# Kernel optimization log

Measured on AMD Instinct MI355X. Metric: run time of the kernel, lower is better.

The kernel has to match this reference:

```python
import jax, jax.numpy as jnp
import numpy as np

N_GENE, N_TRAIN, E = 2500, 16384, 4194304
SRC_DIM, DST_DIM, HID, OUT, NCLS = 2500, 2675, 2500, 2500, 16


def setup_inputs() -> dict:
    key = jax.random.key(0)
    ks = jax.random.split(key, 16)
    s = 0.02
    return {
        "gene_feat": jax.random.normal(ks[0], (N_GENE, SRC_DIM), jnp.float32),
        "train_feat": jax.random.normal(ks[1], (N_TRAIN, DST_DIM), jnp.float32),
        "edge_src": jax.random.randint(ks[2], (E,), 0, N_GENE, jnp.int32),
        "edge_dst": jax.random.randint(ks[3], (E,), 0, N_TRAIN, jnp.int32),
        # conv1: SAGEConv((src=2500, dst=2675) -> 2500, mean)
        "W1_self": jax.random.normal(ks[4], (HID, DST_DIM), jnp.float32) * s,
        "W1_neigh": jax.random.normal(ks[5], (HID, SRC_DIM), jnp.float32) * s,
        "b1": jnp.zeros((HID,), jnp.float32),
        # conv2: SAGEConv(2500 -> 2500, mean); src feats are original gene feats
        "W2_self": jax.random.normal(ks[6], (OUT, HID), jnp.float32) * s,
        "W2_neigh": jax.random.normal(ks[7], (OUT, SRC_DIM), jnp.float32) * s,
        "b2": jnp.zeros((OUT,), jnp.float32),
        # classifier MLP
        "Wc1": jax.random.normal(ks[8], (OUT, OUT), jnp.float32) * s,
        "bc1": jnp.zeros((OUT,), jnp.float32),
        "Wc2": jax.random.normal(ks[9], (NCLS, OUT), jnp.float32) * s,
        "bc2": jnp.zeros((NCLS,), jnp.float32),
    }


def reference(gene_feat, train_feat, edge_src, edge_dst,
              W1_self, W1_neigh, b1, W2_self, W2_neigh, b2,
              Wc1, bc1, Wc2, bc2):
    # Dense incidence-count matrix A[dst, src]: # edges between (dst, src).
    # mean-aggregation over in-edges == (A @ gene_feat) / in_degree.
    A = jnp.zeros((N_TRAIN, N_GENE), jnp.float32).at[edge_dst, edge_src].add(1.0)
    deg = jnp.maximum(A.sum(axis=1, keepdims=True), 1.0)  # zero-in-deg -> neigh term = 0
    mean_src = (A @ gene_feat) / deg                      # [N_train, 2500]

    # conv1 ('connects'): fc_self(dst) + fc_neigh(mean(src)) + bias; then ReLU
    h = jax.nn.relu(train_feat @ W1_self.T + mean_src @ W1_neigh.T + b1)

    # conv2: dst feats = h, src feats = original gene_feat (same graph)
    h2 = jax.nn.relu(h @ W2_self.T + mean_src @ W2_neigh.T + b2)

    # classifier MLP
    return jax.nn.relu(h2 @ Wc1.T + bc1) @ Wc2.T + bc2   # [N_train, 16]
```

## Files before the change

kernel.cpp:

```cpp
#include <hip/hip_runtime.h>
#include <stdint.h>

typedef unsigned short u16;
typedef unsigned int u32;
typedef __attribute__((ext_vector_type(4))) float f32x4;
typedef __attribute__((ext_vector_type(8))) short bf16x8;

#define MROWS 16384
#define NP    2560
#define K1P   2688


__device__ __forceinline__ u16 f2bf(float f) {
    u32 u = __float_as_uint(f);
    u32 r = (u + 0x7fffu + ((u >> 16) & 1u)) >> 16;
    return (u16)r;
}

__device__ __forceinline__ void async_ld16(const void* g, void* l) {
    __builtin_amdgcn_global_load_lds((const __attribute__((address_space(1))) u32*)g,
                                     (__attribute__((address_space(3))) u32*)l,
                                     16, 0, 0);
}


__global__ void cvt_pad(const float* __restrict__ src, u16* __restrict__ dst,
                        int R, int C, int Cp) {
    const int r = blockIdx.x;
    u16* drow = dst + (size_t)r * Cp;
    if (r < R) {
        const float* srow = src + (size_t)r * C;
        for (int c = threadIdx.x; c < Cp; c += blockDim.x)
            drow[c] = (c < C) ? f2bf(srow[c]) : (u16)0;
    } else {
        for (int c = threadIdx.x; c < Cp; c += blockDim.x) drow[c] = 0;
    }
}

__global__ void pad_vec(const float* __restrict__ src, float* __restrict__ dst,
                        int n, int np) {
    int i = blockIdx.x * blockDim.x + threadIdx.x;
    if (i < np) dst[i] = (i < n) ? src[i] : 0.f;
}

__global__ void transpose_cvt(const float* __restrict__ src, u16* __restrict__ dst) {
    __shared__ float t[64][65];
    const int n0 = blockIdx.x * 64;
    const int k0 = blockIdx.y * 64;
    const int tx = threadIdx.x, ty = threadIdx.y;
    for (int i = ty; i < 64; i += 4) {
        int k = k0 + i, n = n0 + tx;
        t[i][tx] = (k < 2500 && n < 2500) ? src[(size_t)k * 2500 + n] : 0.f;
    }
    __syncthreads();
    for (int i = ty; i < 64; i += 4)
        dst[(size_t)(n0 + i) * NP + k0 + tx] = f2bf(t[tx][i]);
}

__global__ void build_counts(const int* __restrict__ esrc, const int* __restrict__ edst,
                             int E, float* __restrict__ acnt) {
    int i = blockIdx.x * blockDim.x + threadIdx.x;
    if (i < E) atomicAdd(&acnt[(size_t)edst[i] * NP + esrc[i]], 1.0f);
}

__global__ void row_rdeg(const float* __restrict__ acnt, float* __restrict__ rdeg) {
    const int row = blockIdx.x;
    const float4* p = (const float4*)(acnt + (size_t)row * NP);
    float s = 0.f;
    for (int i = threadIdx.x; i < NP / 4; i += 64) {
        float4 v = p[i];
        s += v.x + v.y + v.z + v.w;
    }
    #pragma unroll
    for (int off = 32; off > 0; off >>= 1) s += __shfl_down(s, off, 64);
    if (threadIdx.x == 0) rdeg[row] = 1.f / fmaxf(s, 1.f);
}

template<bool PAIR2, bool BIAS_RELU>
__global__ __launch_bounds__(256) void gemm_bt(
    const u16* __restrict__ A1, const u16* __restrict__ B1, int K1,
    const u16* __restrict__ A2, const u16* __restrict__ B2, int K2,
    const float* __restrict__ epi, u16* __restrict__ C, int N)
{
    __shared__ __align__(16) u16 lA[128 * 64];
    __shared__ __align__(16) u16 lB[128 * 64];

    const int tid  = threadIdx.x;
    const int bm   = blockIdx.y * 128;
    const int bn   = blockIdx.x * 128;
    const int wave = tid >> 6;
    const int lane = tid & 63;
    const int wr   = (wave >> 1) << 6;
    const int wc   = (wave & 1) << 6;
    const int lrow = lane & 15;
    const int lkq  = lane >> 4;
    const int xr   = lrow & 7;

    const int sr  = tid >> 3;
    const int sc  = (tid & 7) << 3;
    const int gsw = (((tid & 7) ^ (sr & 7)) << 3);

    f32x4 acc[4][4] = {};

    #pragma unroll
    for (int pair = 0; pair < (PAIR2 ? 2 : 1); ++pair) {
        const u16* A = (PAIR2 && pair) ? A2 : A1;
        const u16* B = (PAIR2 && pair) ? B2 : B1;
        const int  K = (PAIR2 && pair) ? K2 : K1;
        const u16* gA = A + (size_t)(bm + sr) * K + gsw;
        const u16* gB = B + (size_t)(bn + sr) * K + gsw;
        u16* sA = lA + sr * 64 + sc;
        u16* sB = lB + sr * 64 + sc;
        const int nkt = K >> 6;
        for (int kt = 0; kt < nkt; ++kt) {
            __syncthreads();
            const u16* ga = gA + kt * 64;
            const u16* gb = gB + kt * 64;
            #pragma unroll
            for (int i = 0; i < 4; ++i)
                async_ld16(ga + (size_t)i * 32 * K, sA + i * 32 * 64);
            #pragma unroll
            for (int i = 0; i < 4; ++i)
                async_ld16(gb + (size_t)i * 32 * K, sB + i * 32 * 64);
            __syncthreads();
            #pragma unroll
            for (int ks = 0; ks < 2; ++ks) {
                bf16x8 af[4], bfr[4];
                #pragma unroll
                for (int i = 0; i < 4; ++i)
                    af[i] = *(const bf16x8*)(lA + (wr + i * 16 + lrow) * 64 +
                                             (((ks * 4 + lkq) ^ xr) << 3));
                #pragma unroll
                for (int i = 0; i < 4; ++i)
                    bfr[i] = *(const bf16x8*)(lB + (wc + i * 16 + lrow) * 64 +
                                              (((ks * 4 + lkq) ^ xr) << 3));
                #pragma unroll
                for (int mi = 0; mi < 4; ++mi)
                    #pragma unroll
                    for (int ni = 0; ni < 4; ++ni)
                        acc[mi][ni] = __builtin_amdgcn_mfma_f32_16x16x32_bf16(
                            af[mi], bfr[ni], acc[mi][ni], 0, 0, 0);
            }
        }
    }

    const int rbase = bm + wr + lkq * 4;
    const int cbase = bn + wc + lrow;
    if (BIAS_RELU) {
        #pragma unroll
        for (int ni = 0; ni < 4; ++ni) {
            const float bv = epi[cbase + ni * 16];
            #pragma unroll
            for (int mi = 0; mi < 4; ++mi)
                #pragma unroll
                for (int r = 0; r < 4; ++r) {
                    float v = acc[mi][ni][r] + bv;
                    v = fmaxf(v, 0.f);
                    C[(size_t)(rbase + mi * 16 + r) * N + cbase + ni * 16] = f2bf(v);
                }
        }
    } else {
        #pragma unroll
        for (int mi = 0; mi < 4; ++mi)
            #pragma unroll
            for (int r = 0; r < 4; ++r) {
                const float sv = epi[rbase + mi * 16 + r];
                #pragma unroll
                for (int ni = 0; ni < 4; ++ni)
                    C[(size_t)(rbase + mi * 16 + r) * N + cbase + ni * 16] =
                        f2bf(acc[mi][ni][r] * sv);
            }
    }
}

__device__ __forceinline__ float bfdot2(u32 a, u32 b, float acc) {
    float al = __uint_as_float(a << 16), ah = __uint_as_float(a & 0xffff0000u);
    float bl = __uint_as_float(b << 16), bh = __uint_as_float(b & 0xffff0000u);
    return fmaf(ah, bh, fmaf(al, bl, acc));
}

__global__ __launch_bounds__(256) void gemm_cls(
    const u16* __restrict__ hc, const u16* __restrict__ Wc2,
    const float* __restrict__ bc2, float* __restrict__ out)
{
    const int c = threadIdx.x & 15;
    const int r = threadIdx.x >> 4;
    const int row = blockIdx.x * 16 + r;
    const uint4* hp = (const uint4*)(hc + (size_t)row * NP);
    const uint4* wp = (const uint4*)(Wc2 + (size_t)c * NP);
    float acc = 0.f;
    #pragma unroll 4
    for (int i = 0; i < NP / 8; ++i) {
        uint4 a = hp[i], b = wp[i];
        acc = bfdot2(a.x, b.x, acc);
        acc = bfdot2(a.y, b.y, acc);
        acc = bfdot2(a.z, b.z, acc);
        acc = bfdot2(a.w, b.w, acc);
    }
    out[(size_t)row * 16 + c] = acc + bc2[c];
}


extern "C" void kernel_launch(void* const* d_in, const int* in_sizes, int n_in,
                              void* d_out, int out_size, void* d_ws, size_t ws_size,
                              hipStream_t stream) {
    const float* gene  = (const float*)d_in[0];
    const float* train = (const float*)d_in[1];
    const int*   esrc  = (const int*)d_in[2];
    const int*   edst  = (const int*)d_in[3];
    const float* W1s   = (const float*)d_in[4];
    const float* W1n   = (const float*)d_in[5];
    const float* b1    = (const float*)d_in[6];
    const float* W2s   = (const float*)d_in[7];
    const float* W2n   = (const float*)d_in[8];
    const float* b2    = (const float*)d_in[9];
    const float* Wc1   = (const float*)d_in[10];
    const float* bc1   = (const float*)d_in[11];
    const float* Wc2   = (const float*)d_in[12];
    const float* bc2   = (const float*)d_in[13];
    const int E = in_sizes[2];

    char* ws = (char*)d_ws;
    const size_t o_acnt  = 0;
    const size_t o_acntb = 167772160;
    const size_t o_mean  = 251658240;
    const size_t o_train = 335544320;
    const size_t o_w1s   = 423624704;
    const size_t o_w1n   = 437387264;
    const size_t o_w2s   = 450494464;
    const size_t o_w2n   = 463601664;
    const size_t o_wc1   = 476708864;
    const size_t o_gft   = 489816064;
    const size_t o_wc2   = 502923264;
    const size_t o_b1    = 503005184;
    const size_t o_b2    = 503015424;
    const size_t o_bc1   = 503025664;
    const size_t o_rdeg  = 503035904;

    float* ACNT = (float*)(ws + o_acnt);
    u16* ACNTB  = (u16*)(ws + o_acntb);
    u16* MEAN   = (u16*)(ws + o_mean);
    u16* TRAINB = (u16*)(ws + o_train);
    u16* W1S    = (u16*)(ws + o_w1s);
    u16* W1N    = (u16*)(ws + o_w1n);
    u16* W2S    = (u16*)(ws + o_w2s);
    u16* W2N    = (u16*)(ws + o_w2n);
    u16* WC1    = (u16*)(ws + o_wc1);
    u16* GFT    = (u16*)(ws + o_gft);
    u16* WC2    = (u16*)(ws + o_wc2);
    float* B1   = (float*)(ws + o_b1);
    float* B2   = (float*)(ws + o_b2);
    float* BC1  = (float*)(ws + o_bc1);
    float* RDEG = (float*)(ws + o_rdeg);
    u16* H  = (u16*)(ws + o_acnt);
    u16* H2 = (u16*)(ws + o_acntb);
    u16* HC = (u16*)(ws + o_mean);

    hipMemsetAsync(ACNT, 0, (size_t)MROWS * NP * 4, stream);
    build_counts<<<(E + 255) / 256, 256, 0, stream>>>(esrc, edst, E, ACNT);
    row_rdeg<<<MROWS, 64, 0, stream>>>(ACNT, RDEG);

    cvt_pad<<<MROWS, 256, 0, stream>>>(ACNT, ACNTB, MROWS, NP, NP);
    cvt_pad<<<MROWS, 256, 0, stream>>>(train, TRAINB, MROWS, 2675, K1P);
    cvt_pad<<<NP, 256, 0, stream>>>(W1s, W1S, 2500, 2675, K1P);
    cvt_pad<<<NP, 256, 0, stream>>>(W1n, W1N, 2500, 2500, NP);
    cvt_pad<<<NP, 256, 0, stream>>>(W2s, W2S, 2500, 2500, NP);
    cvt_pad<<<NP, 256, 0, stream>>>(W2n, W2N, 2500, 2500, NP);
    cvt_pad<<<NP, 256, 0, stream>>>(Wc1, WC1, 2500, 2500, NP);
    cvt_pad<<<16, 256, 0, stream>>>(Wc2, WC2, 16, 2500, NP);
    transpose_cvt<<<dim3(NP / 64, NP / 64), dim3(64, 4), 0, stream>>>(gene, GFT);
    pad_vec<<<(NP + 255) / 256, 256, 0, stream>>>(b1, B1, 2500, NP);
    pad_vec<<<(NP + 255) / 256, 256, 0, stream>>>(b2, B2, 2500, NP);
    pad_vec<<<(NP + 255) / 256, 256, 0, stream>>>(bc1, BC1, 2500, NP);

    const dim3 ggrid(NP / 128, MROWS / 128);
    gemm_bt<false, false><<<ggrid, 256, 0, stream>>>(
        ACNTB, GFT, NP, nullptr, nullptr, 0, RDEG, MEAN, NP);
    gemm_bt<true, true><<<ggrid, 256, 0, stream>>>(
        TRAINB, W1S, K1P, MEAN, W1N, NP, B1, H, NP);
    gemm_bt<true, true><<<ggrid, 256, 0, stream>>>(
        H, W2S, NP, MEAN, W2N, NP, B2, H2, NP);
    gemm_bt<false, true><<<ggrid, 256, 0, stream>>>(
        H2, WC1, NP, nullptr, nullptr, 0, BC1, HC, NP);
    gemm_cls<<<MROWS / 16, 256, 0, stream>>>(HC, WC2, bc2, (float*)d_out);
}
```

Measured before the change: 2.575 ms.

## Replace 128x128 GEMM with double-buffered 256x256 pipelined MFMA kernel

Replaces the 128x128-tile, 256-thread GEMM with a 256x256-tile, 512-thread kernel. It double-buffers the LDS tiles and interleaves async global-to-LDS staging with quadrant-wise MFMA groups using explicit barriers, waitcnt and setprio. It also adds workgroup index swizzling for L2 locality and hand-written ds_read_b128 addressing. The aim is to hide load latency and raise arithmetic intensity per tile, at the cost of heavy register use (acc[8][4]) and fragile manual scheduling. The loop processes K tiles in pairs, so it assumes an even tile count.

```diff
diff --git a/kernel.cpp b/kernel.cpp
--- a/kernel.cpp
+++ b/kernel.cpp
@@ -21,6 +21,10 @@
     __builtin_amdgcn_global_load_lds((const __attribute__((address_space(1))) u32*)g,
                                      (__attribute__((address_space(3))) u32*)l,
                                      16, 0, 0);
+}
+
+__device__ __forceinline__ u32 lds_b(const void* p) {
+    return (u32)(uintptr_t)(const __attribute__((address_space(3))) void*)p;
 }
 
 
@@ -76,73 +80,132 @@
     if (threadIdx.x == 0) rdeg[row] = 1.f / fmaxf(s, 1.f);
 }
 
+
+#define DSR(dst, ad, off) \
+    asm volatile("ds_read_b128 %0, %1 offset:%2" : "=v"(dst) : "v"(ad), "i"(off))
+
+#define RD_A(BUF, QM) do { \
+    DSR(a[0][0], adA0, (BUF)*32768 + (QM)*8192 + 0);    \
+    DSR(a[0][1], adA1, (BUF)*32768 + (QM)*8192 + 0);    \
+    DSR(a[1][0], adA0, (BUF)*32768 + (QM)*8192 + 2048); \
+    DSR(a[1][1], adA1, (BUF)*32768 + (QM)*8192 + 2048); \
+    DSR(a[2][0], adA0, (BUF)*32768 + (QM)*8192 + 4096); \
+    DSR(a[2][1], adA1, (BUF)*32768 + (QM)*8192 + 4096); \
+    DSR(a[3][0], adA0, (BUF)*32768 + (QM)*8192 + 6144); \
+    DSR(a[3][1], adA1, (BUF)*32768 + (QM)*8192 + 6144); \
+} while (0)
+
+#define RD_B(BUF) do { \
+    DSR(b[0][0], adB0, (BUF)*32768 + 0);    \
+    DSR(b[0][1], adB1, (BUF)*32768 + 0);    \
+    DSR(b[1][0], adB0, (BUF)*32768 + 2048); \
+    DSR(b[1][1], adB1, (BUF)*32768 + 2048); \
+    DSR(b[2][0], adB0, (BUF)*32768 + 4096); \
+    DSR(b[2][1], adB1, (BUF)*32768 + 4096); \
+    DSR(b[3][0], adB0, (BUF)*32768 + 6144); \
+    DSR(b[3][1], adB1, (BUF)*32768 + 6144); \
+} while (0)
+
+#define MFMA_Q(QM, QN) do { \
+    asm volatile("s_waitcnt lgkmcnt(0)" ::: "memory"); \
+    __builtin_amdgcn_sched_barrier(0); \
+    __builtin_amdgcn_s_setprio(1); \
+    _Pragma("unroll") \
+    for (int mi_ = 0; mi_ < 4; ++mi_) { \
+        _Pragma("unroll") \
+        for (int ni_ = 0; ni_ < 2; ++ni_) { \
+            f32x4 c_ = acc[(QM)*4 + mi_][(QN)*2 + ni_]; \
+            c_ = __builtin_amdgcn_mfma_f32_16x16x32_bf16(a[mi_][0], b[(QN)*2 + ni_][0], c_, 0, 0, 0); \
+            c_ = __builtin_amdgcn_mfma_f32_16x16x32_bf16(a[mi_][1], b[(QN)*2 + ni_][1], c_, 0, 0, 0); \
+            acc[(QM)*4 + mi_][(QN)*2 + ni_] = c_; \
+        } \
+    } \
+    __builtin_amdgcn_s_setprio(0); \
+} while (0)
+
+#define XFEN() asm volatile("" ::: "memory")
+#define XBAR() do { XFEN(); __builtin_amdgcn_s_barrier(); XFEN(); } while (0)
+#define WVM6() asm volatile("s_waitcnt vmcnt(6)" ::: "memory")
+
 template<bool PAIR2, bool BIAS_RELU>
-__global__ __launch_bounds__(256) void gemm_bt(
+__global__ __launch_bounds__(512, 2) void gemm256(
     const u16* __restrict__ A1, const u16* __restrict__ B1, int K1,
     const u16* __restrict__ A2, const u16* __restrict__ B2, int K2,
     const float* __restrict__ epi, u16* __restrict__ C, int N)
 {
-    __shared__ __align__(16) u16 lA[128 * 64];
-    __shared__ __align__(16) u16 lB[128 * 64];
+    __shared__ __align__(16) u16 lA[2 * 256 * 64];
+    __shared__ __align__(16) u16 lB[2 * 256 * 64];
 
     const int tid  = threadIdx.x;
-    const int bm   = blockIdx.y * 128;
-    const int bn   = blockIdx.x * 128;
-    const int wave = tid >> 6;
-    const int lane = tid & 63;
-    const int wr   = (wave >> 1) << 6;
-    const int wc   = (wave & 1) << 6;
-    const int lrow = lane & 15;
-    const int lkq  = lane >> 4;
-    const int xr   = lrow & 7;
-
-    const int sr  = tid >> 3;
-    const int sc  = (tid & 7) << 3;
-    const int gsw = (((tid & 7) ^ (sr & 7)) << 3);
-
-    f32x4 acc[4][4] = {};
-
-    #pragma unroll
-    for (int pair = 0; pair < (PAIR2 ? 2 : 1); ++pair) {
-        const u16* A = (PAIR2 && pair) ? A2 : A1;
-        const u16* B = (PAIR2 && pair) ? B2 : B1;
-        const int  K = (PAIR2 && pair) ? K2 : K1;
-        const u16* gA = A + (size_t)(bm + sr) * K + gsw;
-        const u16* gB = B + (size_t)(bn + sr) * K + gsw;
-        u16* sA = lA + sr * 64 + sc;
-        u16* sB = lB + sr * 64 + sc;
-        const int nkt = K >> 6;
-        for (int kt = 0; kt < nkt; ++kt) {
-            __syncthreads();
-            const u16* ga = gA + kt * 64;
-            const u16* gb = gB + kt * 64;
-            #pragma unroll
-            for (int i = 0; i < 4; ++i)
-                async_ld16(ga + (size_t)i * 32 * K, sA + i * 32 * 64);
-            #pragma unroll
-            for (int i = 0; i < 4; ++i)
-                async_ld16(gb + (size_t)i * 32 * K, sB + i * 32 * 64);
-            __syncthreads();
-            #pragma unroll
-            for (int ks = 0; ks < 2; ++ks) {
-                bf16x8 af[4], bfr[4];
-                #pragma unroll
-                for (int i = 0; i < 4; ++i)
-                    af[i] = *(const bf16x8*)(lA + (wr + i * 16 + lrow) * 64 +
-                                             (((ks * 4 + lkq) ^ xr) << 3));
-                #pragma unroll
-                for (int i = 0; i < 4; ++i)
-                    bfr[i] = *(const bf16x8*)(lB + (wc + i * 16 + lrow) * 64 +
-                                              (((ks * 4 + lkq) ^ xr) << 3));
-                #pragma unroll
-                for (int mi = 0; mi < 4; ++mi)
-                    #pragma unroll
-                    for (int ni = 0; ni < 4; ++ni)
-                        acc[mi][ni] = __builtin_amdgcn_mfma_f32_16x16x32_bf16(
-                            af[mi], bfr[ni], acc[mi][ni], 0, 0, 0);
-            }
-        }
-    }
+    const int nwg  = gridDim.x;
+    const int orig = blockIdx.x;
+    const int swz  = (orig & 7) * (nwg >> 3) + (orig >> 3);
+    const int nt   = N >> 8;
+    const int bm   = (swz / nt) << 8;
+    const int bn   = (swz % nt) << 8;
+
+    const int wave = tid >> 6, lane = tid & 63;
+    const int wr   = (wave >> 2) << 7;
+    const int wc   = (wave & 3) << 6;
+    const int lrow = lane & 15, lkq = (lane >> 4) & 3;
+    const int o0   = ((lkq ^ (lrow & 7)) << 3);
+
+    const u32 adA0 = lds_b(lA + (wr + lrow) * 64 + o0);
+    const u32 adA1 = adA0 ^ 64;
+    const u32 adB0 = lds_b(lB + (wc + lrow) * 64 + o0);
+    const u32 adB1 = adB0 ^ 64;
+
+    const int sr   = tid >> 3;
+    const int pc   = tid & 7;
+    const int swzc = ((pc ^ (sr & 7)) << 3);
+    u16* const dA  = lA + sr * 64 + pc * 8;
+    u16* const dB  = lB + sr * 64 + pc * 8;
+
+    const int nk1 = K1 >> 6;
+    const int nkt = nk1 + (PAIR2 ? (K2 >> 6) : 0);
+
+    f32x4 acc[8][4] = {};
+    bf16x8 a[4][2], b[4][2];
+
+    auto STAGE = [&](int mat, int buf, int half, int kt) {
+        int v = (kt < nkt) ? kt : kt - nkt;
+        const u16* base; int K, ko;
+        if (!PAIR2 || v < nk1) { base = mat ? B1 : A1; K = K1; ko = v << 6; }
+        else                   { base = mat ? B2 : A2; K = K2; ko = (v - nk1) << 6; }
+        const int rb = (mat ? bn : bm) + (half << 7) + sr;
+        u16* d = (mat ? dB : dA) + buf * 16384 + half * 8192;
+        const u16* g = base + (size_t)rb * K + ko + swzc;
+        async_ld16(g, d);
+        async_ld16(g + (size_t)64 * K, d + 4096);
+    };
+
+    STAGE(1, 0, 0, 0); STAGE(1, 0, 1, 0); STAGE(0, 0, 0, 0); STAGE(0, 0, 1, 0);
+    STAGE(1, 1, 0, 1); STAGE(1, 1, 1, 1); STAGE(0, 1, 0, 1);
+    WVM6();
+    XBAR();
+
+    const int niter = nkt >> 1;
+    #pragma unroll 1
+    for (int i = 0; i < niter; ++i) {
+        const int t1 = 2 * i + 1, t2 = 2 * i + 2, t3 = 2 * i + 3;
+        RD_A(0, 0); RD_B(0); STAGE(0, 1, 1, t1);
+        XBAR(); MFMA_Q(0, 0); XBAR();
+        STAGE(1, 0, 0, t2);
+        XBAR(); MFMA_Q(0, 1); XBAR();
+        RD_A(0, 1); STAGE(1, 0, 1, t2);
+        XBAR(); MFMA_Q(1, 1); XBAR();
+        STAGE(0, 0, 0, t2); WVM6();
+        XBAR(); MFMA_Q(1, 0); XBAR();
+        RD_A(1, 0); RD_B(1); STAGE(0, 0, 1, t2);
+        XBAR(); MFMA_Q(0, 0); XBAR();
+        STAGE(1, 1, 0, t3);
+        XBAR(); MFMA_Q(0, 1); XBAR();
+        RD_A(1, 1); STAGE(1, 1, 1, t3);
+        XBAR(); MFMA_Q(1, 1); XBAR();
+        STAGE(0, 1, 0, t3); WVM6();
+        XBAR(); MFMA_Q(1, 0); XBAR();
+    }
+    asm volatile("s_waitcnt vmcnt(0)" ::: "memory");
 
     const int rbase = bm + wr + lkq * 4;
     const int cbase = bn + wc + lrow;
@@ -151,7 +214,7 @@
         for (int ni = 0; ni < 4; ++ni) {
             const float bv = epi[cbase + ni * 16];
             #pragma unroll
-            for (int mi = 0; mi < 4; ++mi)
+            for (int mi = 0; mi < 8; ++mi)
                 #pragma unroll
                 for (int r = 0; r < 4; ++r) {
                     float v = acc[mi][ni][r] + bv;
@@ -161,7 +224,7 @@
         }
     } else {
         #pragma unroll
-        for (int mi = 0; mi < 4; ++mi)
+        for (int mi = 0; mi < 8; ++mi)
             #pragma unroll
             for (int r = 0; r < 4; ++r) {
                 const float sv = epi[rbase + mi * 16 + r];
@@ -273,14 +336,14 @@
     pad_vec<<<(NP + 255) / 256, 256, 0, stream>>>(b2, B2, 2500, NP);
     pad_vec<<<(NP + 255) / 256, 256, 0, stream>>>(bc1, BC1, 2500, NP);
 
-    const dim3 ggrid(NP / 128, MROWS / 128);
-    gemm_bt<false, false><<<ggrid, 256, 0, stream>>>(
+    const int NWG = (NP / 256) * (MROWS / 256);
+    gemm256<false, false><<<NWG, 512, 0, stream>>>(
         ACNTB, GFT, NP, nullptr, nullptr, 0, RDEG, MEAN, NP);
-    gemm_bt<true, true><<<ggrid, 256, 0, stream>>>(
+    gemm256<true, true><<<NWG, 512, 0, stream>>>(
         TRAINB, W1S, K1P, MEAN, W1N, NP, B1, H, NP);
-    gemm_bt<true, true><<<ggrid, 256, 0, stream>>>(
+    gemm256<true, true><<<NWG, 512, 0, stream>>>(
         H, W2S, NP, MEAN, W2N, NP, B2, H2, NP);
-    gemm_bt<false, true><<<ggrid, 256, 0, stream>>>(
+    gemm256<false, true><<<NWG, 512, 0, stream>>>(
         H2, WC1, NP, nullptr, nullptr, 0, BC1, HC, NP);
     gemm_cls<<<MROWS / 16, 256, 0, stream>>>(HC, WC2, bc2, (float*)d_out);
 }
```

After: 2.102 ms. 18.3% less time.
